# Performance work log

Measured on AMD Instinct MI355X. Metric: run time of the kernel, lower is better.

Reference implementation:

```python
import jax, jax.numpy as jnp
import numpy as np

B, S, D, H = 2, 2048, 1024, 16
DK = D // H


def setup_inputs() -> dict:
    key = jax.random.key(0)
    ks = jax.random.split(key, 12)
    scale = 1.0 / np.sqrt(D)
    inp = {
        "query": jax.random.normal(ks[0], (B, S, D), jnp.float32),
        "key": jax.random.normal(ks[1], (B, S, D), jnp.float32),
        "value": jax.random.normal(ks[2], (B, S, D), jnp.float32),
        "mask": jax.random.randint(ks[3], (B, 1, S, S), 0, 2, jnp.int32),
        "Wq": jax.random.normal(ks[4], (D, D), jnp.float32) * scale,
        "bq": jnp.zeros((D,), jnp.float32),
        "Wk": jax.random.normal(ks[5], (D, D), jnp.float32) * scale,
        "bk": jnp.zeros((D,), jnp.float32),
        "Wv": jax.random.normal(ks[6], (D, D), jnp.float32) * scale,
        "bv": jnp.zeros((D,), jnp.float32),
        "Wo": jax.random.normal(ks[7], (D, D), jnp.float32) * scale,
        "bo": jnp.zeros((D,), jnp.float32),
    }
    return inp


def reference(query, key, value, mask, Wq, bq, Wk, bk, Wv, bv, Wo, bo):
    # Linear projections (dropout is identity in eval mode)
    q = query @ Wq + bq          # (B,S,D)
    k = key @ Wk + bk
    v = value @ Wv + bv

    # split heads: (B,S,D) -> (B,H,S,DK)
    def split(x):
        return x.reshape(B, S, H, DK).transpose(0, 2, 1, 3)

    q, k, v = split(q), split(k), split(v)

    scores = jnp.einsum("bhqd,bhkd->bhqk", q, k) / jnp.sqrt(jnp.float32(DK))
    scores = jnp.where(mask == 0, jnp.float32(-1e9), scores)
    p_attn = jax.nn.softmax(scores, axis=-1)   # (B,H,S,S)

    att = jnp.einsum("bhqk,bhkd->bhqd", p_attn, v)  # (B,H,S,DK)
    merged = att.transpose(0, 2, 1, 3).reshape(B, S, D)
    return merged @ Wo + bo
```

## Files before the change

### kernel.cpp

```cpp
#include <hip/hip_runtime.h>
#include <hip/hip_bf16.h>
#include <cstdint>
#include <cstddef>


#define B_ 2
#define S_ 2048
#define D_ 1024
#define H_ 16
#define M_ 4096

typedef unsigned short u16;
typedef __attribute__((ext_vector_type(8))) short bf16x8;
typedef __attribute__((ext_vector_type(8))) unsigned short u16x8;
typedef __attribute__((ext_vector_type(4))) unsigned short u16x4;
typedef __attribute__((ext_vector_type(4))) unsigned int u32x4;
typedef __attribute__((ext_vector_type(4))) float f32x4;
typedef __attribute__((ext_vector_type(4))) int i32x4;

#define QSCALE 0.18033688011112042f

__device__ __forceinline__ u16 f2bf(float f) {
  __hip_bfloat16 h = __float2bfloat16(f);
  return *reinterpret_cast<u16*>(&h);
}

__device__ __forceinline__ unsigned cvtpk(float lo, float hi) {
  unsigned r;
  asm("v_cvt_pk_bf16_f32 %0, %1, %2" : "=v"(r) : "v"(lo), "v"(hi));
  return r;
}

__device__ __forceinline__ void gload_lds16(const void* g, void* l) {
  __builtin_amdgcn_global_load_lds((const __attribute__((address_space(1))) void*)g,
                                   (__attribute__((address_space(3))) void*)l, 16, 0, 0);
}

__global__ __launch_bounds__(256) void k_convert(const float* __restrict__ q, const float* __restrict__ k,
                                                 const float* __restrict__ v,
                                                 u16* __restrict__ xq, u16* __restrict__ xk, u16* __restrict__ xv) {
  int z = blockIdx.y;
  const float* src = (z == 0) ? q : (z == 1) ? k : v;
  u16* dst = (z == 0) ? xq : (z == 1) ? xk : xv;
  size_t i = ((size_t)blockIdx.x * 256 + threadIdx.x) * 8;
  f32x4 a = *(const f32x4*)(src + i);
  f32x4 b = *(const f32x4*)(src + i + 4);
  u16x8 o;
  o[0]=f2bf(a[0]); o[1]=f2bf(a[1]); o[2]=f2bf(a[2]); o[3]=f2bf(a[3]);
  o[4]=f2bf(b[0]); o[5]=f2bf(b[1]); o[6]=f2bf(b[2]); o[7]=f2bf(b[3]);
  *(u16x8*)(dst + i) = o;
}

__global__ __launch_bounds__(256) void k_transposeW(const float* __restrict__ w0, const float* __restrict__ w1,
                                                    const float* __restrict__ w2, const float* __restrict__ w3,
                                                    u16* __restrict__ t0, u16* __restrict__ t1,
                                                    u16* __restrict__ t2, u16* __restrict__ t3) {
  int z = blockIdx.z;
  const float* W = (z==0)?w0:(z==1)?w1:(z==2)?w2:w3;
  u16* Wt = (z==0)?t0:(z==1)?t1:(z==2)?t2:t3;
  __shared__ float tile[32][33];
  int tx = threadIdx.x & 31, ty = threadIdx.x >> 5;
  int bx = blockIdx.x * 32, by = blockIdx.y * 32;
  #pragma unroll
  for (int p = 0; p < 4; ++p)
    tile[ty + p*8][tx] = W[(size_t)(by + ty + p*8) * D_ + bx + tx];
  __syncthreads();
  #pragma unroll
  for (int p = 0; p < 4; ++p)
    Wt[(size_t)(bx + ty + p*8) * D_ + by + tx] = f2bf(tile[tx][ty + p*8]);
}

__global__ __launch_bounds__(256) void k_packmask(const int* __restrict__ mask, unsigned* __restrict__ emask) {
  size_t t = (size_t)blockIdx.x * 256 + threadIdx.x;
  const int* p = mask + t * 64;
  unsigned wds[4] = {0u,0u,0u,0u};
  #pragma unroll
  for (int c = 0; c < 16; ++c) {
    i32x4 v = *(const i32x4*)(p + c*4);
    #pragma unroll
    for (int e = 0; e < 4; ++e) {
      const int k = c*4 + e;
      const int lcw = (k >> 3) & 3;
      const int ni = ((k >> 4) & 2) | ((k >> 2) & 1);
      if (v[e]) wds[lcw] |= 1u << (4*ni + (k & 3));
    }
  }
  unsigned* o = emask + t * 32;
  #pragma unroll
  for (int lc = 0; lc < 4; ++lc) {
    u32x4 e0, e1;
    #pragma unroll
    for (int wd = 0; wd < 4; ++wd) {
      e0[wd] = (((wds[lc] >> (2*wd)) & 1u)   ? 0x0000FFFFu : 0u)
             | (((wds[lc] >> (2*wd+1)) & 1u) ? 0xFFFF0000u : 0u);
      e1[wd] = (((wds[lc] >> (8+2*wd)) & 1u)   ? 0x0000FFFFu : 0u)
             | (((wds[lc] >> (8+2*wd+1)) & 1u) ? 0xFFFF0000u : 0u);
    }
    *(u32x4*)(o + lc*8)     = e0;
    *(u32x4*)(o + lc*8 + 4) = e1;
  }
}

template<int CMODE, int MI, int NI>
__device__ __forceinline__ void gemm_core(const u16* __restrict__ A, const u16* __restrict__ Bt,
                                          const float* __restrict__ bias, void* __restrict__ Cv, float scale) {
  extern __shared__ u16 sm[];
  constexpr int ASZ = MI*32*64;
  u16* As = sm;
  u16* Bs = sm + ASZ;
  const int t = threadIdx.x;
  const int l = t & 63, w = t >> 6;
  const int wr = w >> 1, wc = w & 1;
  const int lr = l & 15, lc = l >> 4;
  const int bm = blockIdx.x, bn = blockIdx.y;
  f32x4 acc[MI][NI];
  #pragma unroll
  for (int i = 0; i < MI; ++i)
    #pragma unroll
    for (int j = 0; j < NI; ++j) { f32x4 z = {0.f,0.f,0.f,0.f}; acc[i][j] = z; }
  const int srow = t >> 3;
  const int blkx = (t & 7) ^ (srow & 7);
  const u16* ga = A  + (size_t)(bm*(MI*32) + srow)*1024 + blkx*8;
  const u16* gb = Bt + (size_t)(bn*(NI*32) + srow)*1024 + blkx*8;
  for (int kt = 0; kt < 16; ++kt) {
    const int ko = kt * 64;
    __syncthreads();
    #pragma unroll
    for (int i = 0; i < MI; ++i)
      gload_lds16(ga + (size_t)(i*32)*1024 + ko, &As[i*2048 + t*8]);
    #pragma unroll
    for (int i = 0; i < NI; ++i)
      gload_lds16(gb + (size_t)(i*32)*1024 + ko, &Bs[i*2048 + t*8]);
    __syncthreads();
    #pragma unroll
    for (int ks = 0; ks < 2; ++ks) {
      bf16x8 af[MI], bfr[NI];
      #pragma unroll
      for (int mi = 0; mi < MI; ++mi)
        af[mi]  = *(const bf16x8*)&As[(wr*(MI*16) + mi*16 + lr)*64 + (((ks*4 + lc) ^ (lr & 7))*8)];
      #pragma unroll
      for (int ni = 0; ni < NI; ++ni)
        bfr[ni] = *(const bf16x8*)&Bs[(wc*(NI*16) + ni*16 + lr)*64 + (((ks*4 + lc) ^ (lr & 7))*8)];
      #pragma unroll
      for (int mi = 0; mi < MI; ++mi)
        #pragma unroll
        for (int ni = 0; ni < NI; ++ni)
          acc[mi][ni] = __builtin_amdgcn_mfma_f32_16x16x32_bf16(af[mi], bfr[ni], acc[mi][ni], 0, 0, 0);
    }
  }
  #pragma unroll
  for (int ni = 0; ni < NI; ++ni) {
    int gcol = bn*(NI*32) + wc*(NI*16) + ni*16 + lr;
    float bv = bias[gcol];
    #pragma unroll
    for (int mi = 0; mi < MI; ++mi) {
      int grow = bm*(MI*32) + wr*(MI*16) + mi*16 + lc*4;
      if (CMODE == 2) {
        u16x4 pk;
        #pragma unroll
        for (int j = 0; j < 4; ++j) pk[j] = f2bf((acc[mi][ni][j] + bv) * scale);
        *(u16x4*)&((u16*)Cv)[(size_t)gcol * M_ + grow] = pk;
      } else {
        #pragma unroll
        for (int j = 0; j < 4; ++j) {
          float v = (acc[mi][ni][j] + bv) * scale;
          if (CMODE == 0) ((u16*)Cv)[(size_t)(grow + j) * 1024 + gcol] = f2bf(v);
          else            ((float*)Cv)[(size_t)(grow + j) * 1024 + gcol] = v;
        }
      }
    }
  }
}

__global__ __launch_bounds__(256) void k_gemm_qkv(const u16* Xq, const u16* Xk, const u16* Xv,
                                                  const u16* Wqt, const u16* Wkt, const u16* Wvt,
                                                  const float* bq, const float* bk, const float* bv,
                                                  u16* Qo, u16* Ko, u16* Vt, float qscale) {
  int z = blockIdx.z;
  if (z == 0)      gemm_core<0,4,4>(Xq, Wqt, bq, Qo, qscale);
  else if (z == 1) gemm_core<0,4,4>(Xk, Wkt, bk, Ko, 1.f);
  else             gemm_core<2,4,4>(Xv, Wvt, bv, Vt, 1.f);
}

__global__ __launch_bounds__(256) void k_gemm_out(const u16* Aatt, const u16* Wot, const float* bo, float* out) {
  gemm_core<1,4,2>(Aatt, Wot, bo, out, 1.f);
}

__global__ __launch_bounds__(256) void k_attn(const u16* __restrict__ Q, const u16* __restrict__ Kb,
                                              const u16* __restrict__ Vt,
                                              const unsigned* __restrict__ emask,
                                              u16* __restrict__ attb) {
  __shared__ u16 Ks[3*4096];
  __shared__ u16 Vs[2*4096];
  const int t = threadIdx.x, l = t & 63, w = t >> 6;
  const int lr = l & 15, lc = l >> 4;
  const int id = blockIdx.x + (blockIdx.y << 5) + (blockIdx.z << 9);
  const int lg = (id & 7) * 128 + (id >> 3);
  const int qt = lg & 31, h = (lg >> 5) & 15, b = lg >> 9;
  const int r0 = t >> 3;
  const int c0 = (t & 7) ^ (r0 & 7);
  const int pr0 = ((r0 & 12) << 1) | ((r0 & 16) >> 2) | (r0 & 3);
  const u16* kp0 = Kb + (size_t)(b*S_ + pr0)*D_ + h*64 + c0*8;
  const u16* vp0 = Vt + (size_t)(h*64 + r0)*M_ + b*S_ + c0*8;

  gload_lds16(Q + (size_t)(b*S_ + qt*64 + r0)*D_      + h*64 + c0*8, &Ks[t*8]);
  gload_lds16(Q + (size_t)(b*S_ + qt*64 + r0 + 32)*D_ + h*64 + c0*8, &Ks[2048 + t*8]);
  __syncthreads();
  const int qrow = w*16 + lr;
  const int sw0 = ((lc     ) ^ (lr & 7)) * 8;
  const int sw1 = ((4 + lc ) ^ (lr & 7)) * 8;
  bf16x8 aq0 = *(const bf16x8*)&Ks[qrow*64 + sw0];
  bf16x8 aq1 = *(const bf16x8*)&Ks[qrow*64 + sw1];
  __syncthreads();
  gload_lds16(kp0,                                 &Ks[t*8]);
  gload_lds16(kp0 + (size_t)32*D_,                 &Ks[2048 + t*8]);
  gload_lds16(vp0,                                 &Vs[t*8]);
  gload_lds16(vp0 + (size_t)32*M_,                 &Vs[2048 + t*8]);
  gload_lds16(kp0 + (size_t)64*D_,                 &Ks[4096 + t*8]);
  gload_lds16(kp0 + (size_t)64*D_ + (size_t)32*D_, &Ks[4096 + 2048 + t*8]);

  const short one_bf = (short)0x3F80;
  const bf16x8 onesf = {one_bf,one_bf,one_bf,one_bf,one_bf,one_bf,one_bf,one_bf};
  f32x4 ls = {0.f,0.f,0.f,0.f};
  f32x4 o[4];
  #pragma unroll
  for (int ni = 0; ni < 4; ++ni) { f32x4 z = {0.f,0.f,0.f,0.f}; o[ni] = z; }
  const unsigned* mkp = emask + (size_t)(b*S_ + qt*64 + qrow)*1024 + lc*8;
  const u16* vpA = vp0;
  const u16* vpB = vp0 + (size_t)32*M_;
  const u16* kpA = kp0;
  const u16* kpB = kp0 + (size_t)32*D_;

#define AITER(N, KC, VC, VN, KNN, KPRE, VPRE, WAITN) {                                 \
    asm volatile("s_waitcnt vmcnt(" #WAITN ")");                                       \
    __builtin_amdgcn_s_barrier();                                                      \
    __builtin_amdgcn_sched_barrier(0);                                                 \
    u32x4 mk0 = *(const u32x4*)(mkp + (N)*32);                                         \
    u32x4 mk1 = *(const u32x4*)(mkp + (N)*32 + 4);                                     \
    if (VPRE) {                                                                        \
      gload_lds16(vpA + ((N)+1)*64, &Vs[(VN)*4096 + t*8]);                             \
      gload_lds16(vpB + ((N)+1)*64, &Vs[(VN)*4096 + 2048 + t*8]);                      \
    }                                                                                  \
    if (KPRE) {                                                                        \
      gload_lds16(kpA + (size_t)((N)+2)*64*D_, &Ks[(KNN)*4096 + t*8]);                 \
      gload_lds16(kpB + (size_t)((N)+2)*64*D_, &Ks[(KNN)*4096 + 2048 + t*8]);          \
    }                                                                                  \
    f32x4 s[4];                                                                        \
    _Pragma("unroll")                                                                  \
    for (int ni = 0; ni < 4; ++ni) { f32x4 z = {0.f,0.f,0.f,0.f}; s[ni] = z; }         \
    __builtin_amdgcn_s_setprio(1);                                                     \
    _Pragma("unroll")                                                                  \
    for (int ni = 0; ni < 4; ++ni) {                                                   \
      bf16x8 bk0 = *(const bf16x8*)&Ks[(KC)*4096 + (ni*16 + lr)*64 + sw0];             \
      bf16x8 bk1 = *(const bf16x8*)&Ks[(KC)*4096 + (ni*16 + lr)*64 + sw1];             \
      s[ni] = __builtin_amdgcn_mfma_f32_16x16x32_bf16(bk0, aq0, s[ni], 0, 0, 0);       \
      s[ni] = __builtin_amdgcn_mfma_f32_16x16x32_bf16(bk1, aq1, s[ni], 0, 0, 0);       \
    }                                                                                  \
    __builtin_amdgcn_s_setprio(0);                                                     \
    _Pragma("unroll")                                                                  \
    for (int ni = 0; ni < 4; ++ni)                                                     \
      _Pragma("unroll")                                                                \
      for (int j = 0; j < 4; ++j)                                                      \
        s[ni][j] = __builtin_amdgcn_exp2f(s[ni][j]);                                   \
    u32x4 pw0, pw1;                                                                    \
    pw0[0] = cvtpk(s[0][0], s[0][1]); pw0[1] = cvtpk(s[0][2], s[0][3]);                \
    pw0[2] = cvtpk(s[1][0], s[1][1]); pw0[3] = cvtpk(s[1][2], s[1][3]);                \
    pw1[0] = cvtpk(s[2][0], s[2][1]); pw1[1] = cvtpk(s[2][2], s[2][3]);                \
    pw1[2] = cvtpk(s[3][0], s[3][1]); pw1[3] = cvtpk(s[3][2], s[3][3]);                \
    pw0 &= mk0;                                                                        \
    pw1 &= mk1;                                                                        \
    bf16x8 pa0 = __builtin_bit_cast(bf16x8, pw0);                                      \
    bf16x8 pa1 = __builtin_bit_cast(bf16x8, pw1);                                      \
    __builtin_amdgcn_s_setprio(1);                                                     \
    ls = __builtin_amdgcn_mfma_f32_16x16x32_bf16(pa0, onesf, ls, 0, 0, 0);             \
    ls = __builtin_amdgcn_mfma_f32_16x16x32_bf16(pa1, onesf, ls, 0, 0, 0);             \
    _Pragma("unroll")                                                                  \
    for (int ni = 0; ni < 4; ++ni) {                                                   \
      bf16x8 bv0 = *(const bf16x8*)&Vs[(VC)*4096 + (ni*16 + lr)*64 + sw0];             \
      o[ni] = __builtin_amdgcn_mfma_f32_16x16x32_bf16(pa0, bv0, o[ni], 0, 0, 0);       \
    }                                                                                  \
    _Pragma("unroll")                                                                  \
    for (int ni = 0; ni < 4; ++ni) {                                                   \
      bf16x8 bv1 = *(const bf16x8*)&Vs[(VC)*4096 + (ni*16 + lr)*64 + sw1];             \
      o[ni] = __builtin_amdgcn_mfma_f32_16x16x32_bf16(pa1, bv1, o[ni], 0, 0, 0);       \
    }                                                                                  \
    __builtin_amdgcn_s_setprio(0);                                                     \
  }

  for (int it = 0; it < 5; ++it) {
    AITER(0, 0,0, 1,2, 1,1, 2);
    AITER(1, 1,1, 0,0, 1,1, 2);
    AITER(2, 2,0, 1,1, 1,1, 2);
    AITER(3, 0,1, 0,2, 1,1, 2);
    AITER(4, 1,0, 1,0, 1,1, 2);
    AITER(5, 2,1, 0,1, 1,1, 2);
    mkp += 6*32;
    vpA += 6*64;            vpB += 6*64;
    kpA += (size_t)6*64*D_; kpB += (size_t)6*64*D_;
  }
  AITER(0, 0,0, 1,0, 0,1, 2);
  AITER(1, 1,1, 0,0, 0,0, 0);
#undef AITER

  float rl[4];
  #pragma unroll
  for (int j = 0; j < 4; ++j) rl[j] = 1.f / ls[j];
  #pragma unroll
  for (int ni = 0; ni < 4; ++ni)
    #pragma unroll
    for (int j = 0; j < 4; ++j) {
      int orow = qt*64 + w*16 + lc*4 + j, dcol = ni*16 + lr;
      attb[(size_t)(b*S_ + orow)*D_ + h*64 + dcol] = f2bf(o[ni][j] * rl[j]);
    }
}

extern "C" void kernel_launch(void* const* d_in, const int* in_sizes, int n_in,
                              void* d_out, int out_size, void* d_ws, size_t ws_size,
                              hipStream_t stream) {
  (void)in_sizes; (void)n_in; (void)out_size; (void)ws_size;
  const float* query = (const float*)d_in[0];
  const float* key   = (const float*)d_in[1];
  const float* value = (const float*)d_in[2];
  const int*   mask  = (const int*)d_in[3];
  const float* Wq = (const float*)d_in[4];
  const float* bq = (const float*)d_in[5];
  const float* Wk = (const float*)d_in[6];
  const float* bk = (const float*)d_in[7];
  const float* Wv = (const float*)d_in[8];
  const float* bv = (const float*)d_in[9];
  const float* Wo = (const float*)d_in[10];
  const float* bo = (const float*)d_in[11];
  float* out = (float*)d_out;
  char* ws = (char*)d_ws;
  const size_t MB = 1024 * 1024;
  u16* Xq  = (u16*)(ws + 0*MB);
  u16* Xk  = (u16*)(ws + 8*MB);
  u16* Xv  = (u16*)(ws + 16*MB);
  u16* Wqt = (u16*)(ws + 24*MB);
  u16* Wkt = (u16*)(ws + 26*MB);
  u16* Wvt = (u16*)(ws + 28*MB);
  u16* Wot = (u16*)(ws + 30*MB);
  u16* Qb  = (u16*)(ws + 32*MB);
  u16* Kb  = (u16*)(ws + 40*MB);
  u16* Vtb = (u16*)(ws + 48*MB);
  unsigned* emask = (unsigned*)(ws + 8*MB);
  u16* attb = (u16*)(ws + 0*MB);

  k_convert  <<<dim3(2048, 3),     256, 0,     stream>>>(query, key, value, Xq, Xk, Xv);
  k_transposeW<<<dim3(32, 32, 4),  256, 0,     stream>>>(Wq, Wk, Wv, Wo, Wqt, Wkt, Wvt, Wot);
  k_gemm_qkv <<<dim3(32, 8, 3),    256, 32768, stream>>>(Xq, Xk, Xv, Wqt, Wkt, Wvt, bq, bk, bv,
                                                         Qb, Kb, Vtb, QSCALE);
  k_packmask <<<dim3(512),         256, 0,     stream>>>(mask, emask);
  k_attn     <<<dim3(32, 16, 2),   256, 0,     stream>>>(Qb, Kb, Vtb, emask, attb);
  k_gemm_out <<<dim3(32, 16),      256, 24576, stream>>>(attb, Wot, bo, out);
}
```

Baseline: 151.1 us.

## Pack attention mask into 16-bit bitmasks and apply them after exp2

The mask is no longer expanded into a 32 MB array of per-element 16-bit masks. It is packed into one 16-bit word per lane per 64-key chunk. The attention kernel loads one u16 per iteration and zeroes masked probabilities with a sign-extended bit-select on the fp32 exp values, instead of ANDing packed bf16 vectors. This cuts mask traffic in both the pack kernel and the attention loop by a large factor, at the cost of a few extra ALU ops per score. The GEMM kernels also gain a min-blocks-per-CU launch bound of 4, and the pack kernel is moved ahead of the QKV GEMM into its own workspace region.

```diff
diff --git a/kernel.cpp b/kernel.cpp
--- a/kernel.cpp
+++ b/kernel.cpp
@@ -70,10 +70,10 @@
     Wt[(size_t)(bx + ty + p*8) * D_ + by + tx] = f2bf(tile[tx][ty + p*8]);
 }
 
-__global__ __launch_bounds__(256) void k_packmask(const int* __restrict__ mask, unsigned* __restrict__ emask) {
+__global__ __launch_bounds__(256) void k_packmask(const int* __restrict__ mask, u16* __restrict__ out) {
   size_t t = (size_t)blockIdx.x * 256 + threadIdx.x;
   const int* p = mask + t * 64;
-  unsigned wds[4] = {0u,0u,0u,0u};
+  unsigned wds0 = 0, wds1 = 0, wds2 = 0, wds3 = 0;
   #pragma unroll
   for (int c = 0; c < 16; ++c) {
     i32x4 v = *(const i32x4*)(p + c*4);
@@ -82,23 +82,15 @@
       const int k = c*4 + e;
       const int lcw = (k >> 3) & 3;
       const int ni = ((k >> 4) & 2) | ((k >> 2) & 1);
-      if (v[e]) wds[lcw] |= 1u << (4*ni + (k & 3));
+      const unsigned bit = 1u << (4*ni + (k & 3));
+      if (v[e]) {
+        if (lcw == 0) wds0 |= bit; else if (lcw == 1) wds1 |= bit;
+        else if (lcw == 2) wds2 |= bit; else wds3 |= bit;
+      }
     }
   }
-  unsigned* o = emask + t * 32;
-  #pragma unroll
-  for (int lc = 0; lc < 4; ++lc) {
-    u32x4 e0, e1;
-    #pragma unroll
-    for (int wd = 0; wd < 4; ++wd) {
-      e0[wd] = (((wds[lc] >> (2*wd)) & 1u)   ? 0x0000FFFFu : 0u)
-             | (((wds[lc] >> (2*wd+1)) & 1u) ? 0xFFFF0000u : 0u);
-      e1[wd] = (((wds[lc] >> (8+2*wd)) & 1u)   ? 0x0000FFFFu : 0u)
-             | (((wds[lc] >> (8+2*wd+1)) & 1u) ? 0xFFFF0000u : 0u);
-    }
-    *(u32x4*)(o + lc*8)     = e0;
-    *(u32x4*)(o + lc*8 + 4) = e1;
-  }
+  u16x4 w; w[0] = (u16)wds0; w[1] = (u16)wds1; w[2] = (u16)wds2; w[3] = (u16)wds3;
+  *(u16x4*)(out + t*4) = w;
 }
 
 template<int CMODE, int MI, int NI>
@@ -172,23 +164,23 @@
   }
 }
 
-__global__ __launch_bounds__(256) void k_gemm_qkv(const u16* Xq, const u16* Xk, const u16* Xv,
-                                                  const u16* Wqt, const u16* Wkt, const u16* Wvt,
-                                                  const float* bq, const float* bk, const float* bv,
-                                                  u16* Qo, u16* Ko, u16* Vt, float qscale) {
+__global__ __launch_bounds__(256, 4) void k_gemm_qkv(const u16* Xq, const u16* Xk, const u16* Xv,
+                                                     const u16* Wqt, const u16* Wkt, const u16* Wvt,
+                                                     const float* bq, const float* bk, const float* bv,
+                                                     u16* Qo, u16* Ko, u16* Vt, float qscale) {
   int z = blockIdx.z;
   if (z == 0)      gemm_core<0,4,4>(Xq, Wqt, bq, Qo, qscale);
   else if (z == 1) gemm_core<0,4,4>(Xk, Wkt, bk, Ko, 1.f);
   else             gemm_core<2,4,4>(Xv, Wvt, bv, Vt, 1.f);
 }
 
-__global__ __launch_bounds__(256) void k_gemm_out(const u16* Aatt, const u16* Wot, const float* bo, float* out) {
+__global__ __launch_bounds__(256, 4) void k_gemm_out(const u16* Aatt, const u16* Wot, const float* bo, float* out) {
   gemm_core<1,4,2>(Aatt, Wot, bo, out, 1.f);
 }
 
 __global__ __launch_bounds__(256) void k_attn(const u16* __restrict__ Q, const u16* __restrict__ Kb,
                                               const u16* __restrict__ Vt,
-                                              const unsigned* __restrict__ emask,
+                                              const u16* __restrict__ mbw,
                                               u16* __restrict__ attb) {
   __shared__ u16 Ks[3*4096];
   __shared__ u16 Vs[2*4096];
@@ -225,7 +217,7 @@
   f32x4 o[4];
   #pragma unroll
   for (int ni = 0; ni < 4; ++ni) { f32x4 z = {0.f,0.f,0.f,0.f}; o[ni] = z; }
-  const unsigned* mkp = emask + (size_t)(b*S_ + qt*64 + qrow)*1024 + lc*8;
+  const u16* mkp = mbw + (size_t)(b*S_ + qt*64 + qrow)*128 + lc;
   const u16* vpA = vp0;
   const u16* vpB = vp0 + (size_t)32*M_;
   const u16* kpA = kp0;
@@ -235,8 +227,7 @@
     asm volatile("s_waitcnt vmcnt(" #WAITN ")");                                       \
     __builtin_amdgcn_s_barrier();                                                      \
     __builtin_amdgcn_sched_barrier(0);                                                 \
-    u32x4 mk0 = *(const u32x4*)(mkp + (N)*32);                                         \
-    u32x4 mk1 = *(const u32x4*)(mkp + (N)*32 + 4);                                     \
+    unsigned mw = mkp[(N)*4];                                                          \
     if (VPRE) {                                                                        \
       gload_lds16(vpA + ((N)+1)*64, &Vs[(VN)*4096 + t*8]);                             \
       gload_lds16(vpB + ((N)+1)*64, &Vs[(VN)*4096 + 2048 + t*8]);                      \
@@ -260,15 +251,17 @@
     _Pragma("unroll")                                                                  \
     for (int ni = 0; ni < 4; ++ni)                                                     \
       _Pragma("unroll")                                                                \
-      for (int j = 0; j < 4; ++j)                                                      \
-        s[ni][j] = __builtin_amdgcn_exp2f(s[ni][j]);                                   \
+      for (int j = 0; j < 4; ++j) {                                                    \
+        float pv = __builtin_amdgcn_exp2f(s[ni][j]);                                   \
+        int bmsk = ((int)(mw << (31 - (4*ni + j)))) >> 31;                             \
+        union { float f; int i; } u; u.f = pv; u.i &= bmsk;                            \
+        s[ni][j] = u.f;                                                                \
+      }                                                                                \
     u32x4 pw0, pw1;                                                                    \
     pw0[0] = cvtpk(s[0][0], s[0][1]); pw0[1] = cvtpk(s[0][2], s[0][3]);                \
     pw0[2] = cvtpk(s[1][0], s[1][1]); pw0[3] = cvtpk(s[1][2], s[1][3]);                \
     pw1[0] = cvtpk(s[2][0], s[2][1]); pw1[1] = cvtpk(s[2][2], s[2][3]);                \
     pw1[2] = cvtpk(s[3][0], s[3][1]); pw1[3] = cvtpk(s[3][2], s[3][3]);                \
-    pw0 &= mk0;                                                                        \
-    pw1 &= mk1;                                                                        \
     bf16x8 pa0 = __builtin_bit_cast(bf16x8, pw0);                                      \
     bf16x8 pa1 = __builtin_bit_cast(bf16x8, pw1);                                      \
     __builtin_amdgcn_s_setprio(1);                                                     \
@@ -294,7 +287,7 @@
     AITER(3, 0,1, 0,2, 1,1, 2);
     AITER(4, 1,0, 1,0, 1,1, 2);
     AITER(5, 2,1, 0,1, 1,1, 2);
-    mkp += 6*32;
+    mkp += 24;
     vpA += 6*64;            vpB += 6*64;
     kpA += (size_t)6*64*D_; kpB += (size_t)6*64*D_;
   }
@@ -343,14 +336,14 @@
   u16* Qb  = (u16*)(ws + 32*MB);
   u16* Kb  = (u16*)(ws + 40*MB);
   u16* Vtb = (u16*)(ws + 48*MB);
-  unsigned* emask = (unsigned*)(ws + 8*MB);
+  u16* mbits = (u16*)(ws + 56*MB);
   u16* attb = (u16*)(ws + 0*MB);
 
   k_convert  <<<dim3(2048, 3),     256, 0,     stream>>>(query, key, value, Xq, Xk, Xv);
   k_transposeW<<<dim3(32, 32, 4),  256, 0,     stream>>>(Wq, Wk, Wv, Wo, Wqt, Wkt, Wvt, Wot);
+  k_packmask <<<dim3(512),         256, 0,     stream>>>(mask, mbits);
   k_gemm_qkv <<<dim3(32, 8, 3),    256, 32768, stream>>>(Xq, Xk, Xv, Wqt, Wkt, Wvt, bq, bk, bv,
                                                          Qb, Kb, Vtb, QSCALE);
-  k_packmask <<<dim3(512),         256, 0,     stream>>>(mask, emask);
-  k_attn     <<<dim3(32, 16, 2),   256, 0,     stream>>>(Qb, Kb, Vtb, emask, attb);
+  k_attn     <<<dim3(32, 16, 2),   256, 0,     stream>>>(Qb, Kb, Vtb, mbits, attb);
   k_gemm_out <<<dim3(32, 16),      256, 24576, stream>>>(attb, Wot, bo, out);
 }
```

After: 136.5 us. -9.7%, faster.
